# Performance work log

Measured on AMD Instinct MI355X. Metric: run time of the kernel, lower is better.

## Reference

```python
import jax, jax.numpy as jnp
import numpy as np

N = 100000
E = 3200000
IN_F = 256
OUT_F = 64
ALPHA = 0.2  # LeakyReLU negative slope


def setup_inputs() -> dict:
    key = jax.random.key(0)
    k1, k2, k3, k4 = jax.random.split(key, 4)
    adj = jax.random.randint(k1, (2, E), 0, N, dtype=jnp.int64)
    x = jax.random.normal(k2, (N, IN_F), dtype=jnp.float32)
    # xavier-normal-ish scales
    W_fc = jax.random.normal(k3, (OUT_F, IN_F), dtype=jnp.float32) * (1.414 * np.sqrt(2.0 / (IN_F + OUT_F)))
    b_fc = jnp.zeros((OUT_F,), dtype=jnp.float32)
    a = jax.random.normal(k4, (1, 2 * OUT_F), dtype=jnp.float32) * (1.414 * np.sqrt(2.0 / (1 + 2 * OUT_F)))
    return {"adj": adj, "x": x, "W_fc": W_fc, "b_fc": b_fc, "a": a}


def reference(adj, x, W_fc, b_fc, a):
    src = adj[0]  # [E]
    dst = adj[1]  # [E]
    h = x @ W_fc.T + b_fc                       # [N, OUT_F]
    a1, a2 = a[0, :OUT_F], a[0, OUT_F:]         # split of attention vector
    # e = leakyrelu(a . [h_src || h_dst]) computed without materializing concat
    s1 = h @ a1                                  # [N]
    s2 = h @ a2                                  # [N]
    e = s1[src] + s2[dst]                        # [E]
    e = jnp.where(e > 0, e, ALPHA * e)           # LeakyReLU
    # dgl edge_softmax: softmax over edges grouped by destination node
    m = jax.ops.segment_max(e, dst, num_segments=N)     # [N]
    ex = jnp.exp(e - m[dst])                             # [E]
    denom = jax.ops.segment_sum(ex, dst, num_segments=N) # [N]
    att = ex / denom[dst]                                # [E]
    # SparseTensor(row=src, col=dst, value=att) @ h -> out[src] += att * h[dst]
    h_prime = jax.ops.segment_sum(att[:, None] * h[dst], src, num_segments=N)  # [N, OUT_F]
    return jax.nn.elu(h_prime)  # concat=True branch
```

## Files before the change

kernel.cpp:

```cpp
#include <hip/hip_runtime.h>
#include <math.h>

#define N_NODES 100000
#define N_EDGES 3200000
#define IN_F 256
#define OUT_F 64
#define LRELU_ALPHA 0.2f
#define NBKT 782
#define CAP 4480

typedef unsigned short u16;
typedef __attribute__((ext_vector_type(8))) short short8;
typedef __attribute__((ext_vector_type(4))) float floatx4;

__device__ inline u16 f2bf(float f) {
  unsigned u = __float_as_uint(f);
  u += 0x7FFFu + ((u >> 16) & 1u);
  return (u16)(u >> 16);
}
__device__ inline float bf2f(u16 h) {
  return __uint_as_float(((unsigned)h) << 16);
}

__global__ __launch_bounds__(256) void k_prep(const float* __restrict__ W,
                                              u16* __restrict__ Wbf,
                                              int* __restrict__ sfill,
                                              int* __restrict__ dfill) {
  if (blockIdx.x < 64) {
    int i = blockIdx.x * 256 + threadIdx.x;
    Wbf[i] = f2bf(W[i]);
  } else {
    for (int i = threadIdx.x; i < NBKT; i += 256) {
      sfill[i] = 0;
      dfill[i] = 0;
    }
  }
}

__global__ __launch_bounds__(256) void k_linear(
    const float* __restrict__ x, const u16* __restrict__ Wbf,
    const float* __restrict__ b, const float* __restrict__ a,
    u16* __restrict__ hbf, float* __restrict__ s1, float* __restrict__ s2) {
  __shared__ u16 Wlds[64 * 264];

  const int t = threadIdx.x;
#pragma unroll
  for (int p = 0; p < 8; p++) {
    int c = p * 256 + t;
    int row = c >> 5;
    int kc = (c & 31) * 8;
    *(short8*)&Wlds[row * 264 + kc] = *(const short8*)&Wbf[row * 256 + kc];
  }
  __syncthreads();

  const int w = t >> 6;
  const int lane = t & 63;
  const int col = lane & 15;
  const int q = lane >> 4;
  const int m0 = blockIdx.x * 64 + w * 16;

  floatx4 acc[4];
#pragma unroll
  for (int nt = 0; nt < 4; nt++) acc[nt] = (floatx4){0.f, 0.f, 0.f, 0.f};

  int mrow = m0 + col;
  if (mrow > N_NODES - 1) mrow = N_NODES - 1;
  const float* xrow = x + (size_t)mrow * IN_F + q * 8;

#pragma unroll
  for (int kk = 0; kk < 8; kk++) {
    float4 f0 = *(const float4*)(xrow + kk * 32);
    float4 f1 = *(const float4*)(xrow + kk * 32 + 4);
    short8 af;
    af[0] = (short)f2bf(f0.x);
    af[1] = (short)f2bf(f0.y);
    af[2] = (short)f2bf(f0.z);
    af[3] = (short)f2bf(f0.w);
    af[4] = (short)f2bf(f1.x);
    af[5] = (short)f2bf(f1.y);
    af[6] = (short)f2bf(f1.z);
    af[7] = (short)f2bf(f1.w);
#pragma unroll
    for (int nt = 0; nt < 4; nt++) {
      short8 bfr = *(const short8*)&Wlds[(nt * 16 + col) * 264 + kk * 32 + q * 8];
      acc[nt] = __builtin_amdgcn_mfma_f32_16x16x32_bf16(af, bfr, acc[nt], 0, 0, 0);
    }
  }

  float bv[4], a1v[4], a2v[4];
#pragma unroll
  for (int nt = 0; nt < 4; nt++) {
    bv[nt] = b[nt * 16 + col];
    a1v[nt] = a[nt * 16 + col];
    a2v[nt] = a[OUT_F + nt * 16 + col];
  }
#pragma unroll
  for (int r = 0; r < 4; r++) {
    int node = m0 + q * 4 + r;
    float p1 = 0.f, p2 = 0.f;
#pragma unroll
    for (int nt = 0; nt < 4; nt++) {
      float hv = acc[nt][r] + bv[nt];
      if (node < N_NODES) hbf[(size_t)node * OUT_F + nt * 16 + col] = f2bf(hv);
      p1 = fmaf(hv, a1v[nt], p1);
      p2 = fmaf(hv, a2v[nt], p2);
    }
#pragma unroll
    for (int s = 1; s < 16; s <<= 1) {
      p1 += __shfl_xor(p1, s, 16);
      p2 += __shfl_xor(p2, s, 16);
    }
    if (col == 0 && node < N_NODES) {
      s1[node] = p1;
      s2[node] = p2;
    }
  }
}

#define PBT 512
#define EPT_P 8
#define PEB (PBT * EPT_P)
__global__ __launch_bounds__(PBT) void k_place(
    const int* __restrict__ src, const int* __restrict__ dst,
    const float* __restrict__ s1, const float* __restrict__ s2,
    int* __restrict__ sfill, int* __restrict__ dfill,
    float2* __restrict__ pairS, unsigned* __restrict__ pairD) {
  __shared__ int lc[NBKT];
  __shared__ int ofs[NBKT];
  __shared__ int gbase[NBKT];
  __shared__ int tot;
  __shared__ float2 stage[PEB];
  __shared__ u16 stageB[PEB];

  const int t = threadIdx.x;
  const int side = blockIdx.y;
  const int base = blockIdx.x * PEB + t;

  float ex[EPT_P];
  int key[EPT_P];
  int bk[EPT_P];

  for (int i = t; i < NBKT; i += PBT) lc[i] = 0;
  if (t == 0) tot = 0;
  __syncthreads();

#pragma unroll
  for (int j = 0; j < EPT_P; j++) {
    int e = base + j * PBT;
    if (e < N_EDGES) {
      int s = src[e];
      int d = dst[e];
      float v = s1[s] + s2[d];
      v = v > 0.f ? v : LRELU_ALPHA * v;
      ex[j] = __expf(v);
      if (side == 0) {
        key[j] = d | ((s & 127) << 17);
        bk[j] = s >> 7;
      } else {
        key[j] = d & 127;
        bk[j] = d >> 7;
      }
      atomicAdd(&lc[bk[j]], 1);
    } else {
      bk[j] = -1;
    }
  }
  __syncthreads();

  int* fill = side ? dfill : sfill;
  for (int i = t; i < NBKT; i += PBT) {
    int c = lc[i];
    if (c) {
      gbase[i] = i * CAP + atomicAdd(&fill[i], c);
      ofs[i] = atomicAdd(&tot, c);
    }
  }
  __syncthreads();
  const int nval = tot;
  for (int i = t; i < NBKT; i += PBT) lc[i] = 0;
  __syncthreads();

  if (side == 0) {
#pragma unroll
    for (int j = 0; j < EPT_P; j++) {
      if (bk[j] >= 0) {
        int r = atomicAdd(&lc[bk[j]], 1);
        int idx = ofs[bk[j]] + r;
        stage[idx] = make_float2(ex[j], __int_as_float(key[j]));
        stageB[idx] = (u16)bk[j];
      }
    }
    __syncthreads();
    for (int i = t; i < nval; i += PBT) {
      int bkt = stageB[i];
      pairS[gbase[bkt] + (i - ofs[bkt])] = stage[i];
    }
  } else {
    unsigned* stg32 = (unsigned*)stage;
#pragma unroll
    for (int j = 0; j < EPT_P; j++) {
      if (bk[j] >= 0) {
        int r = atomicAdd(&lc[bk[j]], 1);
        int idx = ofs[bk[j]] + r;
        stg32[idx] = ((unsigned)f2bf(ex[j]) << 16) | (unsigned)key[j];
        stageB[idx] = (u16)bk[j];
      }
    }
    __syncthreads();
    for (int i = t; i < nval; i += PBT) {
      int bkt = stageB[i];
      pairD[gbase[bkt] + (i - ofs[bkt])] = stg32[i];
    }
  }
}

__global__ __launch_bounds__(256) void k_denom(const int* __restrict__ dfill,
                                               const unsigned* __restrict__ pairD,
                                               float* __restrict__ denom_r) {
  __shared__ float lacc[128];
  const int t = threadIdx.x;
  const int bkt = blockIdx.x;
  if (t < 128) lacc[t] = 0.f;
  __syncthreads();
  int beg = bkt * CAP;
  int end = beg + dfill[bkt];
  for (int i = beg + t; i < end; i += 256) {
    unsigned u = pairD[i];
    atomicAdd(&lacc[u & 127], __uint_as_float(u & 0xFFFF0000u));
  }
  __syncthreads();
  if (t < 128) {
    int node = bkt * 128 + t;
    if (node < N_NODES) denom_r[node] = 1.0f / lacc[t];
  }
}

#define SAT 512
__global__ __launch_bounds__(SAT) void k_sortagg(
    const int* __restrict__ sfill, const float2* __restrict__ pairS,
    const float* __restrict__ denom_r, const u16* __restrict__ hbf,
    float* __restrict__ out) {
  __shared__ float2 stg[CAP];
  __shared__ int lcnt[128];
  __shared__ int cur[128];
  __shared__ int nbeg[128];
  __shared__ int nend[128];
  __shared__ int w0tot;
  const int t = threadIdx.x;
  const int bkt = blockIdx.x;

  if (t < 128) lcnt[t] = 0;
  __syncthreads();

  const int gbeg = bkt * CAP;
  const int ne = sfill[bkt];

  for (int i = t; i < ne; i += SAT) {
    int pkv = __float_as_int(pairS[gbeg + i].y);
    atomicAdd(&lcnt[(pkv >> 17) & 127], 1);
  }
  __syncthreads();

  const int lane = t & 63;
  int v = (t < 128) ? lcnt[t] : 0;
  int val = v;
#pragma unroll
  for (int o = 1; o < 64; o <<= 1) {
    int u = __shfl_up(val, o, 64);
    if (lane >= o) val += u;
  }
  if (t == 63) w0tot = val;
  __syncthreads();
  if (t < 128) {
    int excl = val - v + ((t >= 64) ? w0tot : 0);
    cur[t] = excl;
    nbeg[t] = excl;
    nend[t] = excl + v;
  }
  __syncthreads();

  for (int i = t; i < ne; i += SAT) {
    float2 p = pairS[gbeg + i];
    int pkv = __float_as_int(p.y);
    int sl = (pkv >> 17) & 127;
    int d = pkv & 0x1FFFF;
    float att = p.x * denom_r[d];
    int pos = atomicAdd(&cur[sl], 1);
    stg[pos] = make_float2(att, __int_as_float(d));
  }
  __syncthreads();

  const int G = t >> 4;
  const int sl = t & 15;
  for (int nl = G; nl < 128; nl += 32) {
    int node = bkt * 128 + nl;
    int i = nbeg[nl];
    const int e0 = nend[nl];
    float4 acc = make_float4(0.f, 0.f, 0.f, 0.f);
    for (; i + 1 < e0; i += 2) {
      float2 p0 = stg[i];
      float2 p1 = stg[i + 1];
      int d0 = __float_as_int(p0.y);
      int d1 = __float_as_int(p1.y);
      ushort4 q0 = *(const ushort4*)&hbf[(size_t)d0 * OUT_F + sl * 4];
      ushort4 q1 = *(const ushort4*)&hbf[(size_t)d1 * OUT_F + sl * 4];
      acc.x = fmaf(p0.x, bf2f(q0.x), acc.x);
      acc.y = fmaf(p0.x, bf2f(q0.y), acc.y);
      acc.z = fmaf(p0.x, bf2f(q0.z), acc.z);
      acc.w = fmaf(p0.x, bf2f(q0.w), acc.w);
      acc.x = fmaf(p1.x, bf2f(q1.x), acc.x);
      acc.y = fmaf(p1.x, bf2f(q1.y), acc.y);
      acc.z = fmaf(p1.x, bf2f(q1.z), acc.z);
      acc.w = fmaf(p1.x, bf2f(q1.w), acc.w);
    }
    if (i < e0) {
      float2 p = stg[i];
      int d = __float_as_int(p.y);
      ushort4 q = *(const ushort4*)&hbf[(size_t)d * OUT_F + sl * 4];
      acc.x = fmaf(p.x, bf2f(q.x), acc.x);
      acc.y = fmaf(p.x, bf2f(q.y), acc.y);
      acc.z = fmaf(p.x, bf2f(q.z), acc.z);
      acc.w = fmaf(p.x, bf2f(q.w), acc.w);
    }
    if (node < N_NODES) {
      float4 o;
      o.x = acc.x > 0.f ? acc.x : expm1f(acc.x);
      o.y = acc.y > 0.f ? acc.y : expm1f(acc.y);
      o.z = acc.z > 0.f ? acc.z : expm1f(acc.z);
      o.w = acc.w > 0.f ? acc.w : expm1f(acc.w);
      *(float4*)(out + (size_t)node * OUT_F + sl * 4) = o;
    }
  }
}

extern "C" void kernel_launch(void* const* d_in, const int* in_sizes, int n_in,
                              void* d_out, int out_size, void* d_ws,
                              size_t ws_size, hipStream_t stream) {
  const int* adj = (const int*)d_in[0];
  const float* x = (const float*)d_in[1];
  const float* W = (const float*)d_in[2];
  const float* b = (const float*)d_in[3];
  const float* a = (const float*)d_in[4];
  float* out = (float*)d_out;

  float* ws = (float*)d_ws;
  float* s1v = ws;
  float* s2v = ws + 100000;
  float* denom_r = ws + 200000;
  int* sfill = (int*)(ws + 300000);
  int* dfill = (int*)(ws + 300800);
  float2* pairS = (float2*)(ws + 301600);
  unsigned* pairD = (unsigned*)(ws + 7308320);
  u16* hbf = (u16*)(ws + 10811680);
  u16* Wbf = (u16*)(ws + 14011680);

  const int* src = adj;
  const int* dst = adj + N_EDGES;

  k_prep<<<65, 256, 0, stream>>>(W, Wbf, sfill, dfill);
  k_linear<<<(N_NODES + 63) / 64, 256, 0, stream>>>(x, Wbf, b, a, hbf, s1v, s2v);
  k_place<<<dim3((N_EDGES + PEB - 1) / PEB, 2), PBT, 0, stream>>>(
      src, dst, s1v, s2v, sfill, dfill, pairS, pairD);
  k_denom<<<NBKT, 256, 0, stream>>>(dfill, pairD, denom_r);
  k_sortagg<<<NBKT, SAT, 0, stream>>>(sfill, pairS, denom_r, hbf, out);
}
```

Baseline: 365.5 us.

## Coarsen dst buckets, reuse rank from first atomic, split denom, register-cache sort pairs

Destination-side buckets now cover 1024 nodes each (98 buckets) instead of 128, and the denominator kernel splits each bucket across 8 blocks that merge partial sums into a zeroed global array with atomics. The placement kernel keeps the rank returned by the first LDS atomic, so the second counting pass and its barrier are gone. The sort-aggregate kernel moves to 1024 threads, holds its pairs in registers between the count and scatter passes so it reads them once, and applies a fast reciprocal of the denominator at use. The trade-offs are more global atomics, an extra zeroing pass, and higher register pressure in the wider sort-aggregate blocks.

```diff
diff --git a/kernel.cpp b/kernel.cpp
--- a/kernel.cpp
+++ b/kernel.cpp
@@ -8,6 +8,8 @@
 #define LRELU_ALPHA 0.2f
 #define NBKT 782
 #define CAP 4480
+#define NBKTD 98
+#define CAPD 34304
 
 typedef unsigned short u16;
 typedef __attribute__((ext_vector_type(8))) short short8;
@@ -25,14 +27,20 @@
 __global__ __launch_bounds__(256) void k_prep(const float* __restrict__ W,
                                               u16* __restrict__ Wbf,
                                               int* __restrict__ sfill,
-                                              int* __restrict__ dfill) {
+                                              int* __restrict__ dfill,
+                                              float* __restrict__ denom) {
   if (blockIdx.x < 64) {
     int i = blockIdx.x * 256 + threadIdx.x;
     Wbf[i] = f2bf(W[i]);
-  } else {
-    for (int i = threadIdx.x; i < NBKT; i += 256) {
+  } else if (blockIdx.x == 64) {
+    for (int i = threadIdx.x; i < 800; i += 256) {
       sfill[i] = 0;
       dfill[i] = 0;
+    }
+  } else {
+    int i4 = (blockIdx.x - 65) * 256 + threadIdx.x;
+    if (i4 < 25000) {
+      ((float4*)denom)[i4] = make_float4(0.f, 0.f, 0.f, 0.f);
     }
   }
 }
@@ -135,12 +143,14 @@
   const int t = threadIdx.x;
   const int side = blockIdx.y;
   const int base = blockIdx.x * PEB + t;
+  const int nb = side ? NBKTD : NBKT;
 
   float ex[EPT_P];
   int key[EPT_P];
   int bk[EPT_P];
-
-  for (int i = t; i < NBKT; i += PBT) lc[i] = 0;
+  int rk[EPT_P];
+
+  for (int i = t; i < nb; i += PBT) lc[i] = 0;
   if (t == 0) tot = 0;
   __syncthreads();
 
@@ -157,10 +167,10 @@
         key[j] = d | ((s & 127) << 17);
         bk[j] = s >> 7;
       } else {
-        key[j] = d & 127;
-        bk[j] = d >> 7;
+        key[j] = d & 1023;
+        bk[j] = d >> 10;
       }
-      atomicAdd(&lc[bk[j]], 1);
+      rk[j] = atomicAdd(&lc[bk[j]], 1);
     } else {
       bk[j] = -1;
     }
@@ -168,24 +178,22 @@
   __syncthreads();
 
   int* fill = side ? dfill : sfill;
-  for (int i = t; i < NBKT; i += PBT) {
+  const int capb = side ? CAPD : CAP;
+  for (int i = t; i < nb; i += PBT) {
     int c = lc[i];
     if (c) {
-      gbase[i] = i * CAP + atomicAdd(&fill[i], c);
+      gbase[i] = i * capb + atomicAdd(&fill[i], c);
       ofs[i] = atomicAdd(&tot, c);
     }
   }
   __syncthreads();
   const int nval = tot;
-  for (int i = t; i < NBKT; i += PBT) lc[i] = 0;
-  __syncthreads();
 
   if (side == 0) {
 #pragma unroll
     for (int j = 0; j < EPT_P; j++) {
       if (bk[j] >= 0) {
-        int r = atomicAdd(&lc[bk[j]], 1);
-        int idx = ofs[bk[j]] + r;
+        int idx = ofs[bk[j]] + rk[j];
         stage[idx] = make_float2(ex[j], __int_as_float(key[j]));
         stageB[idx] = (u16)bk[j];
       }
@@ -200,8 +208,7 @@
 #pragma unroll
     for (int j = 0; j < EPT_P; j++) {
       if (bk[j] >= 0) {
-        int r = atomicAdd(&lc[bk[j]], 1);
-        int idx = ofs[bk[j]] + r;
+        int idx = ofs[bk[j]] + rk[j];
         stg32[idx] = ((unsigned)f2bf(ex[j]) << 16) | (unsigned)key[j];
         stageB[idx] = (u16)bk[j];
       }
@@ -214,35 +221,41 @@
   }
 }
 
+#define DSUB 8
 __global__ __launch_bounds__(256) void k_denom(const int* __restrict__ dfill,
                                                const unsigned* __restrict__ pairD,
-                                               float* __restrict__ denom_r) {
-  __shared__ float lacc[128];
+                                               float* __restrict__ denom) {
+  __shared__ float lacc[1024];
   const int t = threadIdx.x;
-  const int bkt = blockIdx.x;
-  if (t < 128) lacc[t] = 0.f;
-  __syncthreads();
-  int beg = bkt * CAP;
-  int end = beg + dfill[bkt];
-  for (int i = beg + t; i < end; i += 256) {
+  const int c = blockIdx.x;
+  const int sub = blockIdx.y;
+  for (int i = t; i < 1024; i += 256) lacc[i] = 0.f;
+  __syncthreads();
+  const int fill = dfill[c];
+  const int b0 = c * CAPD + fill * sub / DSUB;
+  const int b1 = c * CAPD + fill * (sub + 1) / DSUB;
+  for (int i = b0 + t; i < b1; i += 256) {
     unsigned u = pairD[i];
-    atomicAdd(&lacc[u & 127], __uint_as_float(u & 0xFFFF0000u));
-  }
-  __syncthreads();
-  if (t < 128) {
-    int node = bkt * 128 + t;
-    if (node < N_NODES) denom_r[node] = 1.0f / lacc[t];
-  }
-}
-
-#define SAT 512
+    atomicAdd(&lacc[u & 1023], __uint_as_float(u & 0xFFFF0000u));
+  }
+  __syncthreads();
+  for (int i = t; i < 1024; i += 256) {
+    float v = lacc[i];
+    if (v != 0.f) {
+      int node = c * 1024 + i;
+      if (node < N_NODES) atomicAdd(&denom[node], v);
+    }
+  }
+}
+
+#define SAT 1024
+#define SMAX 5
 __global__ __launch_bounds__(SAT) void k_sortagg(
     const int* __restrict__ sfill, const float2* __restrict__ pairS,
-    const float* __restrict__ denom_r, const u16* __restrict__ hbf,
+    const float* __restrict__ denom, const u16* __restrict__ hbf,
     float* __restrict__ out) {
   __shared__ float2 stg[CAP];
   __shared__ int lcnt[128];
-  __shared__ int cur[128];
   __shared__ int nbeg[128];
   __shared__ int nend[128];
   __shared__ int w0tot;
@@ -255,9 +268,16 @@
   const int gbeg = bkt * CAP;
   const int ne = sfill[bkt];
 
-  for (int i = t; i < ne; i += SAT) {
-    int pkv = __float_as_int(pairS[gbeg + i].y);
-    atomicAdd(&lcnt[(pkv >> 17) & 127], 1);
+  float2 pr[SMAX];
+  int rk[SMAX];
+#pragma unroll
+  for (int k = 0; k < SMAX; k++) {
+    int i = t + k * SAT;
+    if (i < ne) {
+      float2 p = pairS[gbeg + i];
+      pr[k] = p;
+      rk[k] = atomicAdd(&lcnt[(__float_as_int(p.y) >> 17) & 127], 1);
+    }
   }
   __syncthreads();
 
@@ -273,26 +293,27 @@
   __syncthreads();
   if (t < 128) {
     int excl = val - v + ((t >= 64) ? w0tot : 0);
-    cur[t] = excl;
     nbeg[t] = excl;
     nend[t] = excl + v;
   }
   __syncthreads();
 
-  for (int i = t; i < ne; i += SAT) {
-    float2 p = pairS[gbeg + i];
-    int pkv = __float_as_int(p.y);
-    int sl = (pkv >> 17) & 127;
-    int d = pkv & 0x1FFFF;
-    float att = p.x * denom_r[d];
-    int pos = atomicAdd(&cur[sl], 1);
-    stg[pos] = make_float2(att, __int_as_float(d));
+#pragma unroll
+  for (int k = 0; k < SMAX; k++) {
+    int i = t + k * SAT;
+    if (i < ne) {
+      int pkv = __float_as_int(pr[k].y);
+      int sl = (pkv >> 17) & 127;
+      int d = pkv & 0x1FFFF;
+      float att = pr[k].x * __builtin_amdgcn_rcpf(denom[d]);
+      stg[nbeg[sl] + rk[k]] = make_float2(att, __int_as_float(d));
+    }
   }
   __syncthreads();
 
   const int G = t >> 4;
   const int sl = t & 15;
-  for (int nl = G; nl < 128; nl += 32) {
+  for (int nl = G; nl < 128; nl += 64) {
     int node = bkt * 128 + nl;
     int i = nbeg[nl];
     const int e0 = nend[nl];
@@ -346,21 +367,21 @@
   float* ws = (float*)d_ws;
   float* s1v = ws;
   float* s2v = ws + 100000;
-  float* denom_r = ws + 200000;
+  float* denom = ws + 200000;
   int* sfill = (int*)(ws + 300000);
   int* dfill = (int*)(ws + 300800);
   float2* pairS = (float2*)(ws + 301600);
   unsigned* pairD = (unsigned*)(ws + 7308320);
-  u16* hbf = (u16*)(ws + 10811680);
-  u16* Wbf = (u16*)(ws + 14011680);
+  u16* hbf = (u16*)(ws + 10670112);
+  u16* Wbf = (u16*)(ws + 13870112);
 
   const int* src = adj;
   const int* dst = adj + N_EDGES;
 
-  k_prep<<<65, 256, 0, stream>>>(W, Wbf, sfill, dfill);
+  k_prep<<<165, 256, 0, stream>>>(W, Wbf, sfill, dfill, denom);
   k_linear<<<(N_NODES + 63) / 64, 256, 0, stream>>>(x, Wbf, b, a, hbf, s1v, s2v);
   k_place<<<dim3((N_EDGES + PEB - 1) / PEB, 2), PBT, 0, stream>>>(
       src, dst, s1v, s2v, sfill, dfill, pairS, pairD);
-  k_denom<<<NBKT, 256, 0, stream>>>(dfill, pairD, denom_r);
-  k_sortagg<<<NBKT, SAT, 0, stream>>>(sfill, pairS, denom_r, hbf, out);
-}
+  k_denom<<<dim3(NBKTD, DSUB), 256, 0, stream>>>(dfill, pairD, denom);
+  k_sortagg<<<NBKT, SAT, 0, stream>>>(sfill, pairS, denom, hbf, out);
+}
```

New measurement: 356.3 us. 1.03x faster.
